# Performance work log

Measured on AMD Instinct MI355X. Metric: run time of the kernel, lower is better.

## Reference

```python
import jax, jax.numpy as jnp
import numpy as np
import math

H = 8          # num heads
HID = 768      # LM hidden size
FFN = 3072     # 4 * HID
EOUT = 256     # final embed_dim
EPS = 1e-5


def layernorm(x, g, b):
    m = jnp.mean(x, axis=-1, keepdims=True)
    v = jnp.mean((x - m) ** 2, axis=-1, keepdims=True)
    return (x - m) * jax.lax.rsqrt(v + EPS) * g + b


def _masked_softmax(logits, mask):
    # logits: (b, h, s); mask: (b, s) bool
    logits = jnp.where(mask[:, None, :], logits, -10000.0)
    return jax.nn.softmax(logits, axis=-1)


def fast_attention(x, mask, wq, bq, wk, bk, wv, bv, wo, bo):
    b, s, e = x.shape
    d = e // H
    scale = math.sqrt(d)
    # (b, h, s, d)
    q = (x @ wq + bq).reshape(b, s, H, d).transpose(0, 2, 1, 3)
    k = (x @ wk + bk).reshape(b, s, H, d).transpose(0, 2, 1, 3)
    v = (x @ wv + bv).reshape(b, s, H, d).transpose(0, 2, 1, 3)
    q_w = _masked_softmax(q.sum(-1) / scale, mask)            # (b,h,s)
    q_global = jnp.einsum('bhs,bhsd->bhd', q_w, q)            # (b,h,d)
    k_w = _masked_softmax(jnp.einsum('bhsd,bhd->bhs', k, q_global), mask)
    k_global = jnp.einsum('bhs,bhsd->bhd', k_w, k)
    v_w = _masked_softmax(jnp.einsum('bhsd,bhd->bhs', q, k_global), mask)
    attn_out = v_w[..., None] * v                              # (b,h,s,d)
    attn_out = attn_out.transpose(0, 2, 1, 3).reshape(b, s, e)
    return attn_out @ wo + bo


def fast_pooling(x, mask, wq, bq, wk, bk, wv, bv, wo, bo, ng, nb):
    b, s, e = x.shape
    d = e // H
    scale = math.sqrt(d)
    q = (x @ wq + bq).reshape(b, s, H, d).transpose(0, 2, 1, 3)
    k = (x @ wk + bk).reshape(b, s, H, d).transpose(0, 2, 1, 3)
    v = (x @ wv + bv).reshape(b, s, H, d).transpose(0, 2, 1, 3)
    q_w = _masked_softmax(q.sum(-1) / scale, mask)
    q_global = jnp.einsum('bhs,bhsd->bhd', q_w, q)
    k_w = _masked_softmax(jnp.einsum('bhsd,bhd->bhs', k, q_global), mask)
    k_global = jnp.einsum('bhs,bhsd->bhd', k_w, k)
    v_w = _masked_softmax(jnp.einsum('bhsd,bhd->bhs', q, k_global), mask)
    v_global = jnp.einsum('bhs,bhsd->bhd', v_w, v)            # (b,h,d)
    fused = jnp.concatenate([q_global, v_global], axis=-1)    # (b,h,2d)
    # torch: fused.transpose(1,2).view(b, 2e)  -> layout (b, 2d, h) flattened
    fused = jnp.swapaxes(fused, 1, 2).reshape(b, 2 * e)
    out = fused @ wo + bo
    residual = jnp.swapaxes(q_global, 1, 2).reshape(b, e)
    return layernorm(out + residual, ng, nb)


def setup_inputs() -> dict:
    key = jax.random.key(0)
    ks = iter(jax.random.split(key, 64))
    B, S = 1024, 64

    def w(shape, scale=0.02):
        return jax.random.normal(next(ks), shape, dtype=jnp.float32) * scale

    inp = {
        'token_states': jax.random.normal(next(ks), (B, S, HID), dtype=jnp.float32),
        'attention_mask': jnp.ones((B, S), dtype=jnp.int32),
        # FastformerBlock (1 layer)
        'l_n1_g': jnp.ones((HID,), jnp.float32), 'l_n1_b': jnp.zeros((HID,), jnp.float32),
        'l_wq': w((HID, HID)), 'l_bq': jnp.zeros((HID,), jnp.float32),
        'l_wk': w((HID, HID)), 'l_bk': jnp.zeros((HID,), jnp.float32),
        'l_wv': w((HID, HID)), 'l_bv': jnp.zeros((HID,), jnp.float32),
        'l_wo': w((HID, HID)), 'l_bo': jnp.zeros((HID,), jnp.float32),
        'l_n2_g': jnp.ones((HID,), jnp.float32), 'l_n2_b': jnp.zeros((HID,), jnp.float32),
        'l_w1': w((HID, FFN)), 'l_b1': jnp.zeros((FFN,), jnp.float32),
        'l_w2': w((FFN, HID)), 'l_b2': jnp.zeros((HID,), jnp.float32),
        # FastformerPooling
        'p_wq': w((HID, HID)), 'p_bq': jnp.zeros((HID,), jnp.float32),
        'p_wk': w((HID, HID)), 'p_bk': jnp.zeros((HID,), jnp.float32),
        'p_wv': w((HID, HID)), 'p_bv': jnp.zeros((HID,), jnp.float32),
        'p_wo': w((2 * HID, HID)), 'p_bo': jnp.zeros((HID,), jnp.float32),
        'p_ng': jnp.ones((HID,), jnp.float32), 'p_nb': jnp.zeros((HID,), jnp.float32),
        # token_norm, proj, out_norm
        'tn_g': jnp.ones((HID,), jnp.float32), 'tn_b': jnp.zeros((HID,), jnp.float32),
        'proj_w': w((HID, EOUT)), 'proj_b': jnp.zeros((EOUT,), jnp.float32),
        'on_g': jnp.ones((EOUT,), jnp.float32), 'on_b': jnp.zeros((EOUT,), jnp.float32),
    }
    return inp


def reference(token_states, attention_mask,
              l_n1_g, l_n1_b, l_wq, l_bq, l_wk, l_bk, l_wv, l_bv, l_wo, l_bo,
              l_n2_g, l_n2_b, l_w1, l_b1, l_w2, l_b2,
              p_wq, p_bq, p_wk, p_bk, p_wv, p_bv, p_wo, p_bo, p_ng, p_nb,
              tn_g, tn_b, proj_w, proj_b, on_g, on_b):
    mask = attention_mask != 0
    x = token_states
    # FastformerBlock
    x = x + fast_attention(layernorm(x, l_n1_g, l_n1_b), mask,
                           l_wq, l_bq, l_wk, l_bk, l_wv, l_bv, l_wo, l_bo)
    h = layernorm(x, l_n2_g, l_n2_b)
    x = x + (jax.nn.gelu(h @ l_w1 + l_b1, approximate=False) @ l_w2 + l_b2)
    # Pooling + head
    pooled = fast_pooling(x, mask, p_wq, p_bq, p_wk, p_bk, p_wv, p_bv,
                          p_wo, p_bo, p_ng, p_nb)
    pooled = layernorm(pooled, tn_g, tn_b)
    news_vec = pooled @ proj_w + proj_b
    return layernorm(news_vec, on_g, on_b)
```

## Files before the change

### kernel.cpp

```cpp
#include <hip/hip_runtime.h>
#include <math.h>

#define NHEAD 8
#define HID   768
#define FFND  3072
#define EOUTD 256
#define BATCH 1024
#define TOK   (BATCH*64)

#define EPI_RESF  1
#define EPI_RESB  2
#define EPI_GELU  4
#define EPI_OUTF  8
#define EPI_OUTB  16

typedef __attribute__((ext_vector_type(8))) short short8;
typedef __attribute__((ext_vector_type(4))) float f32x4;

#define AS1 __attribute__((address_space(1)))
#define AS3 __attribute__((address_space(3)))

__device__ __forceinline__ void async16(const void* g, void* l) {
  __builtin_amdgcn_global_load_lds(
      (AS1 unsigned int*)(unsigned long long)g,
      (AS3 unsigned int*)(unsigned int)(unsigned long long)l,
      16, 0, 0);
}

__device__ __forceinline__ float bf2f(unsigned short u) {
  union { unsigned int i; float f; } c; c.i = ((unsigned int)u) << 16; return c.f;
}
__device__ __forceinline__ unsigned short f2bf(float f) {
  union { float f; unsigned int i; } c; c.f = f;
  unsigned int x = c.i + 0x7fffu + ((c.i >> 16) & 1u);
  return (unsigned short)(x >> 16);
}
__device__ __forceinline__ float wsum(float v) {
#pragma unroll
  for (int o = 32; o > 0; o >>= 1) v += __shfl_xor(v, o);
  return v;
}
__device__ __forceinline__ float gelu_f(float v) {
  const float z = fabsf(v) * 0.70710678118654752f;
  const float t = 1.0f / (1.0f + 0.3275911f * z);
  const float poly = t * (0.254829592f + t * (-0.284496736f +
                     t * (1.421413741f + t * (-1.453152027f + t * 1.061405429f))));
  float erfv = 1.0f - poly * __expf(-z * z);
  erfv = (v < 0.f) ? -erfv : erfv;
  return 0.5f * v * (1.0f + erfv);
}

#define SBAR() { __builtin_amdgcn_s_barrier(); asm volatile("" ::: "memory"); }
#define WAITV(n) asm volatile("s_waitcnt vmcnt(" #n ")" ::: "memory")

template<int EPI>
__global__ __launch_bounds__(256, 3) void gemm_k(
    const unsigned short* __restrict__ A, const unsigned short* __restrict__ Wt,
    const float* __restrict__ bias,
    const float* __restrict__ residF, const unsigned short* __restrict__ residB,
    float* __restrict__ outF, unsigned short* __restrict__ outB,
    int M, int N, int K)
{
  __shared__ unsigned short lA[128 * 64];
  __shared__ unsigned short lB[128 * 64];
  const int tid  = threadIdx.x;

  const int nT  = N >> 7;
  const int per = gridDim.x >> 3;
  const int tile = (blockIdx.x & 7) * per + (blockIdx.x >> 3);
  int m_idx = tile / nT;
  int n_idx = tile - m_idx * nT;
  if (m_idx & 1) n_idx = nT - 1 - n_idx;
  const int n0 = n_idx * 128;
  const int m0 = m_idx * 128;

  const int lane = tid & 63;
  const int wid  = tid >> 6;
  const int wm   = wid & 1, wn = wid >> 1;
  const int m16  = lane & 15, quad = lane >> 4;

  f32x4 zero = {0.0f, 0.0f, 0.0f, 0.0f};
  f32x4 acc[4][4];
#pragma unroll
  for (int i = 0; i < 4; i++)
#pragma unroll
    for (int j = 0; j < 4; j++) acc[i][j] = zero;

  long aoff[4], boff[4];
#pragma unroll
  for (int j = 0; j < 4; j++) {
    const int L = tid + j * 256;
    const int row = L >> 3;
    const int kc  = (L & 7) ^ (row & 7);
    aoff[j] = (long)(m0 + row) * K + kc * 8;
    boff[j] = (long)(n0 + row) * K + kc * 8;
  }

  for (int k0 = 0; k0 < K; k0 += 64) {
#pragma unroll
    for (int j = 0; j < 4; j++)
      async16(A + aoff[j] + k0, lA + (size_t)(j * 256 + wid * 64) * 8);
#pragma unroll
    for (int j = 0; j < 4; j++)
      async16(Wt + boff[j] + k0, lB + (size_t)(j * 256 + wid * 64) * 8);
    __syncthreads();
#pragma unroll
    for (int s = 0; s < 2; s++) {
      short8 af[4], bfr[4];
#pragma unroll
      for (int mi = 0; mi < 4; mi++) {
        const int row = wm * 64 + mi * 16 + m16;
        const int kc  = (s * 4 + quad) ^ (row & 7);
        af[mi] = *(const short8*)(lA + row * 64 + kc * 8);
      }
#pragma unroll
      for (int ni = 0; ni < 4; ni++) {
        const int row = wn * 64 + ni * 16 + m16;
        const int kc  = (s * 4 + quad) ^ (row & 7);
        bfr[ni] = *(const short8*)(lB + row * 64 + kc * 8);
      }
#pragma unroll
      for (int mi = 0; mi < 4; mi++)
#pragma unroll
        for (int ni = 0; ni < 4; ni++)
          acc[mi][ni] = __builtin_amdgcn_mfma_f32_16x16x32_bf16(bfr[ni], af[mi], acc[mi][ni], 0, 0, 0);
    }
    __syncthreads();
  }

#pragma unroll
  for (int mi = 0; mi < 4; mi++) {
    const int m = m0 + wm * 64 + mi * 16 + m16;
    const long rb = (long)m * N;
#pragma unroll
    for (int ni = 0; ni < 4; ni++) {
      const int nb = n0 + wn * 64 + ni * 16 + quad * 4;
      f32x4 v = acc[mi][ni];
      const f32x4 bi = *(const f32x4*)(bias + nb);
#pragma unroll
      for (int r = 0; r < 4; r++) v[r] += bi[r];
      if (EPI & EPI_RESF) {
        const f32x4 rf = *(const f32x4*)(residF + rb + nb);
#pragma unroll
        for (int r = 0; r < 4; r++) v[r] += rf[r];
      }
      if (EPI & EPI_RESB) {
        const unsigned long long rv = *(const unsigned long long*)(residB + rb + nb);
#pragma unroll
        for (int r = 0; r < 4; r++) v[r] += bf2f((unsigned short)(rv >> (16 * r)));
      }
      if (EPI & EPI_GELU) {
#pragma unroll
        for (int r = 0; r < 4; r++) v[r] = gelu_f(v[r]);
      }
      if (EPI & EPI_OUTF) *(f32x4*)(outF + rb + nb) = v;
      if (EPI & EPI_OUTB) {
        unsigned long long o = 0;
#pragma unroll
        for (int r = 0; r < 4; r++) o |= (unsigned long long)f2bf(v[r]) << (16 * r);
        *(unsigned long long*)(outB + rb + nb) = o;
      }
    }
  }
}

template<int EPI>
__global__ __launch_bounds__(512, 2) void gemm256_k(
    const unsigned short* __restrict__ A, const unsigned short* __restrict__ Wt,
    const float* __restrict__ bias,
    const float* __restrict__ residF, const unsigned short* __restrict__ residB,
    float* __restrict__ outF, unsigned short* __restrict__ outB,
    int M, int N, int K)
{
  extern __shared__ unsigned short lds[];
  unsigned short* lA = lds;
  unsigned short* lB = lds + 32768;

  const int tid  = threadIdx.x;
  const int lane = tid & 63;
  const int wid  = tid >> 6;

  const int nT  = N >> 8;
  const int per = gridDim.x >> 3;
  const int tile = (blockIdx.x & 7) * per + (blockIdx.x >> 3);
  int m_idx = tile / nT;
  int n_idx = tile - m_idx * nT;
  if (m_idx & 1) n_idx = nT - 1 - n_idx;
  const int m0 = m_idx << 8, n0 = n_idx << 8;

  const int wm = wid >> 2, wn = wid & 3;
  const int m16 = lane & 15, quad = lane >> 4;

  const int r_lo = lane >> 3;
  const int kcg  = (lane & 7) ^ r_lo;
  long aoffj[2], boffj[2];
  int  ldsoj[2];
#pragma unroll
  for (int j = 0; j < 2; ++j) {
    const int rr = (j * 8 + wid) * 8 + r_lo;
    aoffj[j] = (long)(m0 + rr) * K + kcg * 8;
    boffj[j] = (long)(n0 + rr) * K + kcg * 8;
    ldsoj[j] = (j * 8 + wid) * 512;
  }

  auto stA = [&](int c, int hh, int t) {
    async16(A + aoffj[0] + (long)hh * 128 * K + t * 64, lA + c * 16384 + hh * 8192 + ldsoj[0]);
    async16(A + aoffj[1] + (long)hh * 128 * K + t * 64, lA + c * 16384 + hh * 8192 + ldsoj[1]);
  };
  auto stB = [&](int c, int hh, int t) {
    async16(Wt + boffj[0] + (long)hh * 128 * K + t * 64, lB + c * 16384 + hh * 8192 + ldsoj[0]);
    async16(Wt + boffj[1] + (long)hh * 128 * K + t * 64, lB + c * 16384 + hh * 8192 + ldsoj[1]);
  };

  const int xsw = m16 & 7;
  const int kx0 = ((0 + quad) ^ xsw) * 8;
  const int kx1 = ((4 + quad) ^ xsw) * 8;

  f32x4 zero = {0.f, 0.f, 0.f, 0.f};
  f32x4 acc[8][4];
#pragma unroll
  for (int i = 0; i < 8; i++)
#pragma unroll
    for (int j = 0; j < 4; j++) acc[i][j] = zero;

  short8 af[4][2], bf[4][2];
  auto ldA = [&](int c, int mh) {
#pragma unroll
    for (int mi = 0; mi < 4; ++mi) {
      const unsigned short* base = lA + c * 16384 + (wm * 128 + (mh * 4 + mi) * 16 + m16) * 64;
      af[mi][0] = *(const short8*)(base + kx0);
      af[mi][1] = *(const short8*)(base + kx1);
    }
  };
  auto ldB = [&](int c, int nh) {
#pragma unroll
    for (int nn = 0; nn < 2; ++nn) {
      const unsigned short* base = lB + c * 16384 + (wn * 64 + (nh * 2 + nn) * 16 + m16) * 64;
      bf[nh * 2 + nn][0] = *(const short8*)(base + kx0);
      bf[nh * 2 + nn][1] = *(const short8*)(base + kx1);
    }
  };
  auto mmaq = [&](int mh, int nh) {
    __builtin_amdgcn_s_setprio(1);
#pragma unroll
    for (int ks = 0; ks < 2; ++ks)
#pragma unroll
      for (int mi = 0; mi < 4; ++mi)
#pragma unroll
        for (int nn = 0; nn < 2; ++nn)
          acc[mh * 4 + mi][nh * 2 + nn] = __builtin_amdgcn_mfma_f32_16x16x32_bf16(
              bf[nh * 2 + nn][ks], af[mi][ks], acc[mh * 4 + mi][nh * 2 + nn], 0, 0, 0);
    __builtin_amdgcn_s_setprio(0);
  };

  const int NI = K >> 7;

  stA(0, 0, 0); stA(0, 1, 0); stB(0, 0, 0); stB(0, 1, 0);
  stB(1, 0, 1); stB(1, 1, 1);
  WAITV(4);
  SBAR();

  for (int i = 0; i < NI - 1; ++i) {
    const int t1 = 2 * i + 1, s0 = 2 * i + 2, s1 = 2 * i + 3;
    ldA(0, 0); ldB(0, 0);
    stA(1, 0, t1);
    SBAR(); mmaq(0, 0); SBAR();
    ldB(0, 1);
    stA(1, 1, t1);
    SBAR(); mmaq(0, 1); SBAR();
    ldA(0, 1);
    stB(0, 0, s0);
    SBAR(); mmaq(1, 1); SBAR();
    stB(0, 1, s0);
    WAITV(4);
    SBAR(); mmaq(1, 0); SBAR();
    ldA(1, 0); ldB(1, 0);
    stA(0, 0, s0);
    SBAR(); mmaq(0, 0); SBAR();
    ldB(1, 1);
    stA(0, 1, s0);
    SBAR(); mmaq(0, 1); SBAR();
    ldA(1, 1);
    stB(1, 0, s1);
    SBAR(); mmaq(1, 1); SBAR();
    stB(1, 1, s1);
    WAITV(4);
    SBAR(); mmaq(1, 0); SBAR();
  }
  {
    const int t1 = 2 * NI - 1;
    ldA(0, 0); ldB(0, 0);
    stA(1, 0, t1);
    SBAR(); mmaq(0, 0); SBAR();
    ldB(0, 1);
    stA(1, 1, t1);
    SBAR(); mmaq(0, 1); SBAR();
    ldA(0, 1);
    SBAR(); mmaq(1, 1); SBAR();
    WAITV(0);
    SBAR(); mmaq(1, 0); SBAR();
    ldA(1, 0); ldB(1, 0);
    SBAR(); mmaq(0, 0); SBAR();
    ldB(1, 1);
    SBAR(); mmaq(0, 1); SBAR();
    ldA(1, 1);
    SBAR(); mmaq(1, 1); SBAR();
    mmaq(1, 0);
  }

#pragma unroll
  for (int mi = 0; mi < 8; ++mi) {
    const int m = m0 + wm * 128 + mi * 16 + m16;
    const long rb = (long)m * N;
#pragma unroll
    for (int ni = 0; ni < 4; ++ni) {
      const int nb = n0 + wn * 64 + ni * 16 + quad * 4;
      f32x4 v = acc[mi][ni];
      const f32x4 bi = *(const f32x4*)(bias + nb);
#pragma unroll
      for (int r = 0; r < 4; r++) v[r] += bi[r];
      if (EPI & EPI_RESF) {
        const f32x4 rf = *(const f32x4*)(residF + rb + nb);
#pragma unroll
        for (int r = 0; r < 4; r++) v[r] += rf[r];
      }
      if (EPI & EPI_RESB) {
        const unsigned long long rv = *(const unsigned long long*)(residB + rb + nb);
#pragma unroll
        for (int r = 0; r < 4; r++) v[r] += bf2f((unsigned short)(rv >> (16 * r)));
      }
      if (EPI & EPI_GELU) {
#pragma unroll
        for (int r = 0; r < 4; r++) v[r] = gelu_f(v[r]);
      }
      if (EPI & EPI_OUTF) *(f32x4*)(outF + rb + nb) = v;
      if (EPI & EPI_OUTB) {
        unsigned long long o = 0;
#pragma unroll
        for (int r = 0; r < 4; r++) o |= (unsigned long long)f2bf(v[r]) << (16 * r);
        *(unsigned long long*)(outB + rb + nb) = o;
      }
    }
  }
}

template<bool POOL>
__global__ __launch_bounds__(256) void fastattn2_k(
    const unsigned short* __restrict__ Q,
    const unsigned short* __restrict__ Kx,
    const unsigned short* __restrict__ V,
    int ld,
    const int* __restrict__ mask,
    unsigned short* __restrict__ attnO,
    unsigned short* __restrict__ fused,
    float* __restrict__ qres)
{
  const int lane = threadIdx.x & 63;
  const int wid  = threadIdx.x >> 6;
  const int gw   = blockIdx.x * 4 + wid;
  const int b = gw >> 3, h = gw & 7;
  const int c = lane & 15, quad = lane >> 4;
  const unsigned short* Qp = Q  + (long)b * 64 * ld + h * 96;
  const unsigned short* Kp = Kx + (long)b * 64 * ld + h * 96;
  const unsigned short* Vp = V  + (long)b * 64 * ld + h * 96;
  const float mval = (mask[b * 64 + lane] != 0) ? 1.0f : 0.0f;

  f32x4 G[4][4];
  f32x4 zero = {0.f, 0.f, 0.f, 0.f};
#pragma unroll
  for (int mi = 0; mi < 4; mi++)
#pragma unroll
    for (int ni = 0; ni < 4; ni++) G[mi][ni] = zero;
  float ql[4] = {0.f, 0.f, 0.f, 0.f};

#pragma unroll
  for (int kc = 0; kc < 3; kc++) {
    const int dcol = kc * 32 + quad * 8;
    short8 afr[4], bfr[4];
#pragma unroll
    for (int mi = 0; mi < 4; mi++)
      afr[mi] = *(const short8*)(Kp + (long)(mi * 16 + c) * ld + dcol);
#pragma unroll
    for (int ni = 0; ni < 4; ni++)
      bfr[ni] = *(const short8*)(Qp + (long)(ni * 16 + c) * ld + dcol);
#pragma unroll
    for (int ni = 0; ni < 4; ni++) {
      float t = 0.f;
#pragma unroll
      for (int j = 0; j < 8; j++) t += bf2f((unsigned short)bfr[ni][j]);
      ql[ni] += t;
    }
#pragma unroll
    for (int mi = 0; mi < 4; mi++)
#pragma unroll
      for (int ni = 0; ni < 4; ni++)
        G[mi][ni] = __builtin_amdgcn_mfma_f32_16x16x32_bf16(afr[mi], bfr[ni], G[mi][ni], 0, 0, 0);
  }
#pragma unroll
  for (int ni = 0; ni < 4; ni++) {
    ql[ni] += __shfl_xor(ql[ni], 16);
    ql[ni] += __shfl_xor(ql[ni], 32);
  }

  float qw[4];
  {
    float lg[4], mx = -3.4e38f;
#pragma unroll
    for (int ni = 0; ni < 4; ni++) {
      const float mk = __shfl(mval, ni * 16 + c);
      lg[ni] = (mk > 0.5f) ? ql[ni] * 0.102062072615966f : -10000.0f;
      mx = fmaxf(mx, lg[ni]);
    }
#pragma unroll
    for (int o = 1; o <= 8; o <<= 1) mx = fmaxf(mx, __shfl_xor(mx, o));
    float se = 0.f;
#pragma unroll
    for (int ni = 0; ni < 4; ni++) { qw[ni] = expf(lg[ni] - mx); se += qw[ni]; }
#pragma unroll
    for (int o = 1; o <= 8; o <<= 1) se += __shfl_xor(se, o);
    const float inv = 1.0f / se;
#pragma unroll
    for (int ni = 0; ni < 4; ni++) qw[ni] *= inv;
  }

  float kw[16];
#pragma unroll
  for (int mi = 0; mi < 4; mi++)
#pragma unroll
    for (int r = 0; r < 4; r++) {
      float a = 0.f;
#pragma unroll
      for (int ni = 0; ni < 4; ni++) a += G[mi][ni][r] * qw[ni];
      kw[mi * 4 + r] = a;
    }
#pragma unroll
  for (int i = 0; i < 16; i++)
#pragma unroll
    for (int o = 1; o <= 8; o <<= 1) kw[i] += __shfl_xor(kw[i], o);

  {
    float mx2 = -3.4e38f;
#pragma unroll
    for (int i = 0; i < 16; i++) {
      const int mi = i >> 2, r = i & 3;
      const float mk = __shfl(mval, mi * 16 + quad * 4 + r);
      kw[i] = (mk > 0.5f) ? kw[i] : -10000.0f;
      mx2 = fmaxf(mx2, kw[i]);
    }
    mx2 = fmaxf(mx2, __shfl_xor(mx2, 16));
    mx2 = fmaxf(mx2, __shfl_xor(mx2, 32));
    float se2 = 0.f;
#pragma unroll
    for (int i = 0; i < 16; i++) { kw[i] = expf(kw[i] - mx2); se2 += kw[i]; }
    se2 += __shfl_xor(se2, 16);
    se2 += __shfl_xor(se2, 32);
    const float inv = 1.0f / se2;
#pragma unroll
    for (int i = 0; i < 16; i++) kw[i] *= inv;
  }

  float vw[4];
  {
    float vl[4] = {0.f, 0.f, 0.f, 0.f};
#pragma unroll
    for (int ni = 0; ni < 4; ni++) {
#pragma unroll
      for (int mi = 0; mi < 4; mi++)
#pragma unroll
        for (int r = 0; r < 4; r++) vl[ni] += G[mi][ni][r] * kw[mi * 4 + r];
      vl[ni] += __shfl_xor(vl[ni], 16);
      vl[ni] += __shfl_xor(vl[ni], 32);
    }
    float mx = -3.4e38f;
#pragma unroll
    for (int ni = 0; ni < 4; ni++) {
      const float mk = __shfl(mval, ni * 16 + c);
      vl[ni] = (mk > 0.5f) ? vl[ni] : -10000.0f;
      mx = fmaxf(mx, vl[ni]);
    }
#pragma unroll
    for (int o = 1; o <= 8; o <<= 1) mx = fmaxf(mx, __shfl_xor(mx, o));
    float se = 0.f;
#pragma unroll
    for (int ni = 0; ni < 4; ni++) { vw[ni] = expf(vl[ni] - mx); se += vw[ni]; }
#pragma unroll
    for (int o = 1; o <= 8; o <<= 1) se += __shfl_xor(se, o);
    const float inv = 1.0f / se;
#pragma unroll
    for (int ni = 0; ni < 4; ni++) vw[ni] *= inv;
  }

  if (!POOL) {
    __shared__ float swv[4][64];
    if (quad == 0) {
#pragma unroll
      for (int ni = 0; ni < 4; ni++) swv[wid][ni * 16 + c] = vw[ni];
    }
    __syncthreads();
    unsigned short* Op = attnO + (long)b * 64 * 768 + h * 96;
#pragma unroll
    for (int it = 0; it < 12; it++) {
      const int idx = it * 64 + lane;
      const int s = idx / 12, cw = idx % 12;
      short8 v = *(const short8*)(Vp + (long)s * ld + cw * 8);
      const float w = swv[wid][s];
      short8 o;
#pragma unroll
      for (int j = 0; j < 8; j++) o[j] = (short)f2bf(w * bf2f((unsigned short)v[j]));
      *(short8*)(Op + (long)s * 768 + cw * 8) = o;
    }
  } else {
    float qg[24], vg[24];
#pragma unroll
    for (int kc = 0; kc < 3; kc++) {
      const int dcol = kc * 32 + quad * 8;
      short8 fq[4], fv[4];
#pragma unroll
      for (int ni = 0; ni < 4; ni++) {
        fq[ni] = *(const short8*)(Qp + (long)(ni * 16 + c) * ld + dcol);
        fv[ni] = *(const short8*)(Vp + (long)(ni * 16 + c) * ld + dcol);
      }
#pragma unroll
      for (int j = 0; j < 8; j++) {
        float aq = 0.f, av = 0.f;
#pragma unroll
        for (int ni = 0; ni < 4; ni++) {
          aq += qw[ni] * bf2f((unsigned short)fq[ni][j]);
          av += vw[ni] * bf2f((unsigned short)fv[ni][j]);
        }
        qg[kc * 8 + j] = aq; vg[kc * 8 + j] = av;
      }
    }
#pragma unroll
    for (int i = 0; i < 24; i++) {
#pragma unroll
      for (int o = 1; o <= 8; o <<= 1) {
        qg[i] += __shfl_xor(qg[i], o);
        vg[i] += __shfl_xor(vg[i], o);
      }
    }
    if (c == 0) {
#pragma unroll
      for (int kc = 0; kc < 3; kc++)
#pragma unroll
        for (int j = 0; j < 8; j++) {
          const int d = kc * 32 + quad * 8 + j;
          const float qv = qg[kc * 8 + j], vv = vg[kc * 8 + j];
          fused[(long)b * 1536 + d * 8 + h]        = f2bf(qv);
          fused[(long)b * 1536 + (96 + d) * 8 + h] = f2bf(vv);
          qres[(long)b * 768 + d * 8 + h] = qv;
        }
    }
  }
}

__global__ __launch_bounds__(256) void ln768_k(
    const float* __restrict__ x, const float* __restrict__ g, const float* __restrict__ b,
    unsigned short* __restrict__ out)
{
  const int tid = threadIdx.x;
  const long row = blockIdx.x;
  const float* xr = x + row * 768;
  const float v0 = xr[tid], v1 = xr[tid + 256], v2 = xr[tid + 512];
  __shared__ float red[4];
  const int wid = tid >> 6, ln = tid & 63;
  float s = wsum(v0 + v1 + v2);
  if (ln == 0) red[wid] = s;
  __syncthreads();
  const float mean = (red[0] + red[1] + red[2] + red[3]) * (1.0f / 768.0f);
  __syncthreads();
  const float d0 = v0 - mean, d1 = v1 - mean, d2 = v2 - mean;
  float q = wsum(d0 * d0 + d1 * d1 + d2 * d2);
  if (ln == 0) red[wid] = q;
  __syncthreads();
  const float var = (red[0] + red[1] + red[2] + red[3]) * (1.0f / 768.0f);
  const float rs = rsqrtf(var + 1e-5f);
  unsigned short* o = out + row * 768;
  o[tid]       = f2bf(d0 * rs * g[tid]       + b[tid]);
  o[tid + 256] = f2bf(d1 * rs * g[tid + 256] + b[tid + 256]);
  o[tid + 512] = f2bf(d2 * rs * g[tid + 512] + b[tid + 512]);
}

__global__ __launch_bounds__(256) void ln768b_k(
    const unsigned short* __restrict__ x, const float* __restrict__ g, const float* __restrict__ b,
    unsigned short* __restrict__ out)
{
  const int tid = threadIdx.x;
  const long row = blockIdx.x;
  const unsigned short* xr = x + row * 768;
  const float v0 = bf2f(xr[tid]), v1 = bf2f(xr[tid + 256]), v2 = bf2f(xr[tid + 512]);
  __shared__ float red[4];
  const int wid = tid >> 6, ln = tid & 63;
  float s = wsum(v0 + v1 + v2);
  if (ln == 0) red[wid] = s;
  __syncthreads();
  const float mean = (red[0] + red[1] + red[2] + red[3]) * (1.0f / 768.0f);
  __syncthreads();
  const float d0 = v0 - mean, d1 = v1 - mean, d2 = v2 - mean;
  float q = wsum(d0 * d0 + d1 * d1 + d2 * d2);
  if (ln == 0) red[wid] = q;
  __syncthreads();
  const float var = (red[0] + red[1] + red[2] + red[3]) * (1.0f / 768.0f);
  const float rs = rsqrtf(var + 1e-5f);
  unsigned short* o = out + row * 768;
  o[tid]       = f2bf(d0 * rs * g[tid]       + b[tid]);
  o[tid + 256] = f2bf(d1 * rs * g[tid + 256] + b[tid + 256]);
  o[tid + 512] = f2bf(d2 * rs * g[tid + 512] + b[tid + 512]);
}

__global__ __launch_bounds__(256) void ln2x_k(
    const float* __restrict__ x,
    const float* __restrict__ g1, const float* __restrict__ b1,
    const float* __restrict__ g2, const float* __restrict__ b2,
    unsigned short* __restrict__ out)
{
  const int tid = threadIdx.x;
  const long row = blockIdx.x;
  const float* xr = x + row * 768;
  const float v0 = xr[tid], v1 = xr[tid + 256], v2 = xr[tid + 512];
  __shared__ float red[4];
  const int wid = tid >> 6, ln = tid & 63;
  float s = wsum(v0 + v1 + v2);
  if (ln == 0) red[wid] = s;
  __syncthreads();
  const float mean = (red[0] + red[1] + red[2] + red[3]) * (1.0f / 768.0f);
  __syncthreads();
  const float d0 = v0 - mean, d1 = v1 - mean, d2 = v2 - mean;
  float q = wsum(d0 * d0 + d1 * d1 + d2 * d2);
  if (ln == 0) red[wid] = q;
  __syncthreads();
  const float var = (red[0] + red[1] + red[2] + red[3]) * (1.0f / 768.0f);
  const float rs = rsqrtf(var + 1e-5f);
  const float y0 = d0 * rs * g1[tid]       + b1[tid];
  const float y1 = d1 * rs * g1[tid + 256] + b1[tid + 256];
  const float y2 = d2 * rs * g1[tid + 512] + b1[tid + 512];
  __syncthreads();
  float s2 = wsum(y0 + y1 + y2);
  if (ln == 0) red[wid] = s2;
  __syncthreads();
  const float mean2 = (red[0] + red[1] + red[2] + red[3]) * (1.0f / 768.0f);
  __syncthreads();
  const float e0 = y0 - mean2, e1 = y1 - mean2, e2 = y2 - mean2;
  float q2 = wsum(e0 * e0 + e1 * e1 + e2 * e2);
  if (ln == 0) red[wid] = q2;
  __syncthreads();
  const float var2 = (red[0] + red[1] + red[2] + red[3]) * (1.0f / 768.0f);
  const float rs2 = rsqrtf(var2 + 1e-5f);
  unsigned short* o = out + row * 768;
  o[tid]       = f2bf(e0 * rs2 * g2[tid]       + b2[tid]);
  o[tid + 256] = f2bf(e1 * rs2 * g2[tid + 256] + b2[tid + 256]);
  o[tid + 512] = f2bf(e2 * rs2 * g2[tid + 512] + b2[tid + 512]);
}

__global__ __launch_bounds__(256) void lnf_k(
    const float* __restrict__ x, const float* __restrict__ g, const float* __restrict__ b,
    float* __restrict__ out)
{
  const int tid = threadIdx.x;
  const long row = blockIdx.x;
  const float v = x[row * 256 + tid];
  __shared__ float red[4];
  const int wid = tid >> 6, ln = tid & 63;
  float s = wsum(v);
  if (ln == 0) red[wid] = s;
  __syncthreads();
  const float mean = (red[0] + red[1] + red[2] + red[3]) * (1.0f / 256.0f);
  __syncthreads();
  const float d = v - mean;
  float q = wsum(d * d);
  if (ln == 0) red[wid] = q;
  __syncthreads();
  const float var = (red[0] + red[1] + red[2] + red[3]) * (1.0f / 256.0f);
  const float rs = rsqrtf(var + 1e-5f);
  out[row * 256 + tid] = d * rs * g[tid] + b[tid];
}

__global__ __launch_bounds__(256) void tcast_k(
    const float* __restrict__ W, unsigned short* __restrict__ Wt, int K, int N)
{
  __shared__ float t[32][33];
  const int tx = threadIdx.x & 31, ty = threadIdx.x >> 5;
  const int n0 = blockIdx.x * 32, k0 = blockIdx.y * 32;
#pragma unroll
  for (int j = 0; j < 32; j += 8)
    t[ty + j][tx] = W[(long)(k0 + ty + j) * N + n0 + tx];
  __syncthreads();
#pragma unroll
  for (int j = 0; j < 32; j += 8)
    Wt[(long)(n0 + ty + j) * K + k0 + tx] = f2bf(t[tx][ty + j]);
}

__global__ __launch_bounds__(256) void cat3_k(
    const float* __restrict__ a, const float* __restrict__ b, const float* __restrict__ c,
    float* __restrict__ dst)
{
  const int i = blockIdx.x * 256 + threadIdx.x;
  dst[i] = (i < 768) ? a[i] : (i < 1536 ? b[i - 768] : c[i - 1536]);
}

extern "C" void kernel_launch(void* const* d_in, const int* in_sizes, int n_in,
                              void* d_out, int out_size, void* d_ws, size_t ws_size,
                              hipStream_t stream)
{
  const float* x    = (const float*)d_in[0];
  const int*   mask = (const int*)d_in[1];
  const float* n1g = (const float*)d_in[2];  const float* n1b = (const float*)d_in[3];
  const float* wq  = (const float*)d_in[4];  const float* bq  = (const float*)d_in[5];
  const float* wk  = (const float*)d_in[6];  const float* bk  = (const float*)d_in[7];
  const float* wv  = (const float*)d_in[8];  const float* bv  = (const float*)d_in[9];
  const float* wo  = (const float*)d_in[10]; const float* bo  = (const float*)d_in[11];
  const float* n2g = (const float*)d_in[12]; const float* n2b = (const float*)d_in[13];
  const float* w1  = (const float*)d_in[14]; const float* b1  = (const float*)d_in[15];
  const float* w2  = (const float*)d_in[16]; const float* b2  = (const float*)d_in[17];
  const float* pwq = (const float*)d_in[18]; const float* pbq = (const float*)d_in[19];
  const float* pwk = (const float*)d_in[20]; const float* pbk = (const float*)d_in[21];
  const float* pwv = (const float*)d_in[22]; const float* pbv = (const float*)d_in[23];
  const float* pwo = (const float*)d_in[24]; const float* pbo = (const float*)d_in[25];
  const float* png = (const float*)d_in[26]; const float* pnb = (const float*)d_in[27];
  const float* tng = (const float*)d_in[28]; const float* tnb = (const float*)d_in[29];
  const float* pjw = (const float*)d_in[30]; const float* pjb = (const float*)d_in[31];
  const float* ong = (const float*)d_in[32]; const float* onb = (const float*)d_in[33];
  float* out = (float*)d_out;

  static int lds_attr_done = 0;
  if (!lds_attr_done) {
    lds_attr_done = 1;
    hipFuncSetAttribute((const void*)gemm256_k<EPI_OUTB>,
                        hipFuncAttributeMaxDynamicSharedMemorySize, 131072);
    hipFuncSetAttribute((const void*)gemm256_k<EPI_OUTB | EPI_RESF>,
                        hipFuncAttributeMaxDynamicSharedMemorySize, 131072);
    hipFuncSetAttribute((const void*)gemm256_k<EPI_OUTB | EPI_GELU>,
                        hipFuncAttributeMaxDynamicSharedMemorySize, 131072);
    hipFuncSetAttribute((const void*)gemm256_k<EPI_OUTB | EPI_RESB>,
                        hipFuncAttributeMaxDynamicSharedMemorySize, 131072);
  }

  char* p = (char*)d_ws;
  auto alloc = [&](size_t n) { void* r = (void*)p; p += (n + 255) & ~(size_t)255; return r; };

  unsigned short* wqkvt = (unsigned short*)alloc((size_t)3 * HID * HID * 2);
  unsigned short* wot   = (unsigned short*)alloc((size_t)HID * HID * 2);
  unsigned short* w1t   = (unsigned short*)alloc((size_t)FFND * HID * 2);
  unsigned short* w2t   = (unsigned short*)alloc((size_t)HID * FFND * 2);
  unsigned short* pqkvt = (unsigned short*)alloc((size_t)3 * HID * HID * 2);
  unsigned short* pwot  = (unsigned short*)alloc((size_t)HID * 2 * HID * 2);
  unsigned short* pjwt  = (unsigned short*)alloc((size_t)EOUTD * HID * 2);
  float*          qkvbias = (float*)alloc((size_t)3 * HID * 4);
  float*          pqkvbias= (float*)alloc((size_t)3 * HID * 4);
  unsigned short* bfA   = (unsigned short*)alloc((size_t)TOK * HID * 2);
  unsigned short* QKVb  = (unsigned short*)alloc((size_t)TOK * 3 * HID * 2);
  unsigned short* bfB   = (unsigned short*)alloc((size_t)TOK * HID * 2);
  unsigned short* x2b   = (unsigned short*)alloc((size_t)TOK * HID * 2);
  unsigned short* fusedb= (unsigned short*)alloc((size_t)BATCH * 2 * HID * 2);
  float*          qresb = (float*)alloc((size_t)BATCH * HID * 4);
  float*          preln = (float*)alloc((size_t)BATCH * HID * 4);
  unsigned short* pooledb=(unsigned short*)alloc((size_t)BATCH * HID * 2);
  float*          news  = (float*)alloc((size_t)BATCH * EOUTD * 4);
  (void)ws_size; (void)in_sizes; (void)n_in; (void)out_size;

  tcast_k<<<dim3(HID/32,  HID/32),  256, 0, stream>>>(wq,  wqkvt,                 HID, HID);
  tcast_k<<<dim3(HID/32,  HID/32),  256, 0, stream>>>(wk,  wqkvt + (size_t)HID*HID,   HID, HID);
  tcast_k<<<dim3(HID/32,  HID/32),  256, 0, stream>>>(wv,  wqkvt + (size_t)2*HID*HID, HID, HID);
  tcast_k<<<dim3(HID/32,  HID/32),  256, 0, stream>>>(wo,  wot,  HID,  HID);
  tcast_k<<<dim3(FFND/32, HID/32),  256, 0, stream>>>(w1,  w1t,  HID,  FFND);
  tcast_k<<<dim3(HID/32,  FFND/32), 256, 0, stream>>>(w2,  w2t,  FFND, HID);
  tcast_k<<<dim3(HID/32,  HID/32),  256, 0, stream>>>(pwq, pqkvt,                 HID, HID);
  tcast_k<<<dim3(HID/32,  HID/32),  256, 0, stream>>>(pwk, pqkvt + (size_t)HID*HID,   HID, HID);
  tcast_k<<<dim3(HID/32,  HID/32),  256, 0, stream>>>(pwv, pqkvt + (size_t)2*HID*HID, HID, HID);
  tcast_k<<<dim3(HID/32,  (2*HID)/32), 256, 0, stream>>>(pwo, pwot, 2*HID, HID);
  tcast_k<<<dim3(EOUTD/32, HID/32), 256, 0, stream>>>(pjw, pjwt, HID,  EOUTD);
  cat3_k<<<9, 256, 0, stream>>>(bq,  bk,  bv,  qkvbias);
  cat3_k<<<9, 256, 0, stream>>>(pbq, pbk, pbv, pqkvbias);

  ln768_k<<<TOK, 256, 0, stream>>>(x, n1g, n1b, bfA);

  gemm256_k<EPI_OUTB><<<(TOK/256)*(3*HID/256), 512, 131072, stream>>>(
      bfA, wqkvt, qkvbias, nullptr, nullptr, nullptr, QKVb, TOK, 3*HID, HID);

  fastattn2_k<false><<<BATCH * NHEAD / 4, 256, 0, stream>>>(
      QKVb, QKVb + HID, QKVb + 2*HID, 3*HID, mask, bfB, nullptr, nullptr);

  gemm256_k<EPI_OUTB | EPI_RESF><<<(TOK/256)*(HID/256), 512, 131072, stream>>>(
      bfB, wot, bo, x, nullptr, nullptr, x2b, TOK, HID, HID);

  ln768b_k<<<TOK, 256, 0, stream>>>(x2b, n2g, n2b, bfA);

  for (int c = 0; c < 2; c++) {
    const size_t ro = (size_t)c * 32768;
    gemm256_k<EPI_OUTB | EPI_GELU><<<(32768/256)*(FFND/256), 512, 131072, stream>>>(
        bfA + ro * HID, w1t, b1, nullptr, nullptr, nullptr, QKVb, 32768, FFND, HID);
    gemm256_k<EPI_OUTB | EPI_RESB><<<(32768/256)*(HID/256), 512, 131072, stream>>>(
        QKVb, w2t, b2, nullptr, x2b + ro * HID, nullptr, bfA + ro * HID, 32768, HID, FFND);
  }

  gemm256_k<EPI_OUTB><<<(TOK/256)*(3*HID/256), 512, 131072, stream>>>(
      bfA, pqkvt, pqkvbias, nullptr, nullptr, nullptr, QKVb, TOK, 3*HID, HID);

  fastattn2_k<true><<<BATCH * NHEAD / 4, 256, 0, stream>>>(
      QKVb, QKVb + HID, QKVb + 2*HID, 3*HID, mask, nullptr, fusedb, qresb);

  gemm_k<EPI_OUTF | EPI_RESF><<<(BATCH/128)*(HID/128), 256, 0, stream>>>(
      fusedb, pwot, pbo, qresb, nullptr, preln, nullptr, BATCH, HID, 2*HID);

  ln2x_k<<<BATCH, 256, 0, stream>>>(preln, png, pnb, tng, tnb, pooledb);

  gemm_k<EPI_OUTF><<<(BATCH/128)*(EOUTD/128), 256, 0, stream>>>(
      pooledb, pjwt, pjb, nullptr, nullptr, news, nullptr, BATCH, EOUTD, HID);

  lnf_k<<<BATCH, 256, 0, stream>>>(news, ong, onb, out);
}
```

Baseline: 2.439 ms.

## Route most GEMMs to 128-tile kernel and hand-schedule LDS reads in 256-tile kernel

Switches the output-projection, both FFN GEMMs and the pooling QKV GEMM from the 256x256 tile kernel with 128KB of dynamic LDS to the 128x128 tile kernel (3 blocks per CU), keeping the 256-tile kernel only for the first QKV GEMM. Inside the 256-tile kernel, LDS fragment loads now go through inline-asm ds_read_b128, followed by an explicit lgkmcnt(0) wait and a scheduling barrier before each MFMA group. The memory clobbers are dropped from the barrier and vmcnt-wait macros. The intent is higher occupancy and better latency hiding for the large GEMMs, at the cost of less data reuse per tile. Removing the memory clobbers risks the compiler reordering memory accesses across the barriers.

Measured after the change: 2.686 ms. +10.1%, slower.

```diff
diff --git a/kernel.cpp b/kernel.cpp
--- a/kernel.cpp
+++ b/kernel.cpp
@@ -25,6 +25,13 @@
       (AS1 unsigned int*)(unsigned long long)g,
       (AS3 unsigned int*)(unsigned int)(unsigned long long)l,
       16, 0, 0);
+}
+
+__device__ __forceinline__ short8 dsr16(const unsigned short* p) {
+  short8 r;
+  const unsigned a = (unsigned)(unsigned long long)p;
+  asm volatile("ds_read_b128 %0, %1" : "=v"(r) : "v"(a));
+  return r;
 }
 
 __device__ __forceinline__ float bf2f(unsigned short u) {
@@ -50,8 +57,9 @@
   return 0.5f * v * (1.0f + erfv);
 }
 
-#define SBAR() { __builtin_amdgcn_s_barrier(); asm volatile("" ::: "memory"); }
-#define WAITV(n) asm volatile("s_waitcnt vmcnt(" #n ")" ::: "memory")
+#define SBAR() __builtin_amdgcn_s_barrier()
+#define WAITV(n) asm volatile("s_waitcnt vmcnt(" #n ")")
+#define LGKM0() { asm volatile("s_waitcnt lgkmcnt(0)"); __builtin_amdgcn_sched_barrier(0); }
 
 template<int EPI>
 __global__ __launch_bounds__(256, 3) void gemm_k(
@@ -228,19 +236,20 @@
 #pragma unroll
     for (int mi = 0; mi < 4; ++mi) {
       const unsigned short* base = lA + c * 16384 + (wm * 128 + (mh * 4 + mi) * 16 + m16) * 64;
-      af[mi][0] = *(const short8*)(base + kx0);
-      af[mi][1] = *(const short8*)(base + kx1);
+      af[mi][0] = dsr16(base + kx0);
+      af[mi][1] = dsr16(base + kx1);
     }
   };
   auto ldB = [&](int c, int nh) {
 #pragma unroll
     for (int nn = 0; nn < 2; ++nn) {
       const unsigned short* base = lB + c * 16384 + (wn * 64 + (nh * 2 + nn) * 16 + m16) * 64;
-      bf[nh * 2 + nn][0] = *(const short8*)(base + kx0);
-      bf[nh * 2 + nn][1] = *(const short8*)(base + kx1);
+      bf[nh * 2 + nn][0] = dsr16(base + kx0);
+      bf[nh * 2 + nn][1] = dsr16(base + kx1);
     }
   };
   auto mmaq = [&](int mh, int nh) {
+    LGKM0();
     __builtin_amdgcn_s_setprio(1);
 #pragma unroll
     for (int ks = 0; ks < 2; ++ks)
@@ -727,12 +736,6 @@
     lds_attr_done = 1;
     hipFuncSetAttribute((const void*)gemm256_k<EPI_OUTB>,
                         hipFuncAttributeMaxDynamicSharedMemorySize, 131072);
-    hipFuncSetAttribute((const void*)gemm256_k<EPI_OUTB | EPI_RESF>,
-                        hipFuncAttributeMaxDynamicSharedMemorySize, 131072);
-    hipFuncSetAttribute((const void*)gemm256_k<EPI_OUTB | EPI_GELU>,
-                        hipFuncAttributeMaxDynamicSharedMemorySize, 131072);
-    hipFuncSetAttribute((const void*)gemm256_k<EPI_OUTB | EPI_RESB>,
-                        hipFuncAttributeMaxDynamicSharedMemorySize, 131072);
   }
 
   char* p = (char*)d_ws;
@@ -780,20 +783,20 @@
   fastattn2_k<false><<<BATCH * NHEAD / 4, 256, 0, stream>>>(
       QKVb, QKVb + HID, QKVb + 2*HID, 3*HID, mask, bfB, nullptr, nullptr);
 
-  gemm256_k<EPI_OUTB | EPI_RESF><<<(TOK/256)*(HID/256), 512, 131072, stream>>>(
+  gemm_k<EPI_OUTB | EPI_RESF><<<(TOK/128)*(HID/128), 256, 0, stream>>>(
       bfB, wot, bo, x, nullptr, nullptr, x2b, TOK, HID, HID);
 
   ln768b_k<<<TOK, 256, 0, stream>>>(x2b, n2g, n2b, bfA);
 
   for (int c = 0; c < 2; c++) {
     const size_t ro = (size_t)c * 32768;
-    gemm256_k<EPI_OUTB | EPI_GELU><<<(32768/256)*(FFND/256), 512, 131072, stream>>>(
+    gemm_k<EPI_OUTB | EPI_GELU><<<(32768/128)*(FFND/128), 256, 0, stream>>>(
         bfA + ro * HID, w1t, b1, nullptr, nullptr, nullptr, QKVb, 32768, FFND, HID);
-    gemm256_k<EPI_OUTB | EPI_RESB><<<(32768/256)*(HID/256), 512, 131072, stream>>>(
+    gemm_k<EPI_OUTB | EPI_RESB><<<(32768/128)*(HID/128), 256, 0, stream>>>(
         QKVb, w2t, b2, nullptr, x2b + ro * HID, nullptr, bfA + ro * HID, 32768, HID, FFND);
   }
 
-  gemm256_k<EPI_OUTB><<<(TOK/256)*(3*HID/256), 512, 131072, stream>>>(
+  gemm_k<EPI_OUTB><<<(TOK/128)*(3*HID/128), 256, 0, stream>>>(
       bfA, pqkvt, pqkvbias, nullptr, nullptr, nullptr, QKVb, TOK, 3*HID, HID);
 
   fastattn2_k<true><<<BATCH * NHEAD / 4, 256, 0, stream>>>(
```
